# Performance work log

Hardware: AMD Instinct MI355X
Metric: run time of the kernel (lower is better)

The kernel has to match this reference:

```python
import jax, jax.numpy as jnp
import numpy as np
import math

HEAD_DIM = 128
N_HEADS = 32
N_KV_HEADS = 8
HIDDEN = 4096
ROPE_BASE = 10000.0


def _rope_cos_sin(position_ids):
    # inv_freq: [D/2]
    inv_freq = 1.0 / (ROPE_BASE ** (jnp.arange(0, HEAD_DIM, 2, dtype=jnp.float32) / HEAD_DIM))
    freqs = position_ids.astype(jnp.float32)[..., None] * inv_freq  # [B,S,D/2]
    emb = jnp.concatenate([freqs, freqs], axis=-1)  # [B,S,D]
    return jnp.cos(emb), jnp.sin(emb)


def _rotate_half(x):
    x1, x2 = jnp.split(x, 2, axis=-1)
    return jnp.concatenate([-x2, x1], axis=-1)


def setup_inputs() -> dict:
    key = jax.random.key(0)
    ks = jax.random.split(key, 5)
    B, S = 1, 2048
    inp = {
        "hidden_states": jax.random.normal(ks[0], (B, S, HIDDEN), dtype=jnp.float32),
        "position_ids": jnp.arange(B * S, dtype=jnp.int32).reshape(B, S),
        "Wq": jax.random.normal(ks[1], (HIDDEN, N_HEADS * HEAD_DIM), dtype=jnp.float32) * 0.02,
        "Wk": jax.random.normal(ks[2], (HIDDEN, N_KV_HEADS * HEAD_DIM), dtype=jnp.float32) * 0.02,
        "Wv": jax.random.normal(ks[3], (HIDDEN, N_KV_HEADS * HEAD_DIM), dtype=jnp.float32) * 0.02,
        "Wo": jax.random.normal(ks[4], (N_HEADS * HEAD_DIM, HIDDEN), dtype=jnp.float32) * 0.02,
    }
    return inp


def reference(hidden_states, position_ids, Wq, Wk, Wv, Wo):
    B, S, _ = hidden_states.shape
    G = N_HEADS // N_KV_HEADS

    q = (hidden_states @ Wq).reshape(B, S, N_HEADS, HEAD_DIM).transpose(0, 2, 1, 3)      # [B,H,S,D]
    k = (hidden_states @ Wk).reshape(B, S, N_KV_HEADS, HEAD_DIM).transpose(0, 2, 1, 3)   # [B,Hkv,S,D]
    v = (hidden_states @ Wv).reshape(B, S, N_KV_HEADS, HEAD_DIM).transpose(0, 2, 1, 3)

    cos, sin = _rope_cos_sin(position_ids)          # [B,S,D]
    cos = cos[:, None, :, :]                         # [B,1,S,D]
    sin = sin[:, None, :, :]
    q = q * cos + _rotate_half(q) * sin
    k = k * cos + _rotate_half(k) * sin

    # GQA head expansion (repeat_interleave over head dim)
    k = jnp.repeat(k, G, axis=1)                     # [B,H,S,D]
    v = jnp.repeat(v, G, axis=1)

    scale = 1.0 / math.sqrt(HEAD_DIM)
    scores = jnp.einsum("bhqd,bhkd->bhqk", q, k) * scale  # [B,H,S,S]
    causal = jnp.triu(jnp.full((S, S), -jnp.inf, dtype=scores.dtype), k=1)
    scores = scores + causal[None, None]
    probs = jax.nn.softmax(scores.astype(jnp.float32), axis=-1).astype(q.dtype)
    ctx = jnp.einsum("bhqk,bhkd->bhqd", probs, v)    # [B,H,S,D]
    ctx = ctx.transpose(0, 2, 1, 3).reshape(B, S, N_HEADS * HEAD_DIM)
    return ctx @ Wo
```

## Files before the change

### kernel.cpp

```cpp
#include <hip/hip_runtime.h>
#include <hip/hip_bf16.h>
#include <math.h>

#define SEQ 2048
#define NHEADS 32
#define NKVH 8
#define HD 128
#define HIDDEN 4096

typedef unsigned short u16;
typedef unsigned int u32;
typedef __attribute__((ext_vector_type(8))) __bf16 bf16x8;
typedef __attribute__((ext_vector_type(4))) float f32x4;
typedef __attribute__((ext_vector_type(16))) float f32x16;
typedef __attribute__((ext_vector_type(4))) u16 u16x4;
typedef __attribute__((ext_vector_type(4))) u32 u32x4;

__device__ __forceinline__ u16 f2bf(float f) {
  u32 u = __builtin_bit_cast(u32, f);
  u32 r = (u + 0x7fffu + ((u >> 16) & 1u)) >> 16;
  return (u16)r;
}
__device__ __forceinline__ float bf2f(u16 h) {
  return __builtin_bit_cast(float, ((u32)h) << 16);
}
__device__ __forceinline__ void gload_lds16(const void* g, void* l) {
  __builtin_amdgcn_global_load_lds(
      (const __attribute__((address_space(1))) u32*)g,
      (__attribute__((address_space(3))) u32*)l, 16, 0, 0);
}

#define BAR __builtin_amdgcn_s_barrier()
#define PRIO1 __builtin_amdgcn_s_setprio(1)
#define PRIO0 __builtin_amdgcn_s_setprio(0)
#define VMW(n) asm volatile("s_waitcnt vmcnt(" #n ")" ::: "memory")

__global__ void __launch_bounds__(256) prep_all(
    const float* __restrict__ hs, u16* __restrict__ Xb,
    const float* __restrict__ Wq, u16* __restrict__ Wqt,
    const float* __restrict__ Wk, u16* __restrict__ Wkt,
    const float* __restrict__ Wv, u16* __restrict__ Wvt) {
  const int bid = blockIdx.x;
  if (bid < 8192) {
    const int i = (bid * 256 + threadIdx.x) * 4;
    const float4 v = *(const float4*)(hs + i);
    u16x4 o;
    o.x = f2bf(v.x); o.y = f2bf(v.y); o.z = f2bf(v.z); o.w = f2bf(v.w);
    *(u16x4*)(Xb + i) = o;
    return;
  }
  __shared__ float tile[64][65];
  const float* src; u16* dst; int C, lc, tb;
  const int b2 = bid - 8192;
  if (b2 < 4096) { src = Wq; dst = Wqt; C = 4096; lc = 6; tb = b2; }
  else if (b2 < 5120) { src = Wk; dst = Wkt; C = 1024; lc = 4; tb = b2 - 4096; }
  else { src = Wv; dst = Wvt; C = 1024; lc = 4; tb = b2 - 5120; }
  const int r0 = (tb >> lc) * 64, c0 = (tb & ((1 << lc) - 1)) * 64;
  const int tx = threadIdx.x & 63, ty = threadIdx.x >> 6;
#pragma unroll
  for (int j = 0; j < 16; ++j)
    tile[ty + j * 4][tx] = src[(size_t)(r0 + ty + j * 4) * C + c0 + tx];
  __syncthreads();
#pragma unroll
  for (int j = 0; j < 16; ++j)
    dst[(size_t)(c0 + ty + j * 4) * 4096 + r0 + tx] = f2bf(tile[tx][ty + j * 4]);
}

__global__ void __launch_bounds__(256) post_qkv(u16* __restrict__ qb, u16* __restrict__ kb,
                                                const u16* __restrict__ vb, u16* __restrict__ vtb,
                                                const int* __restrict__ pos) {
  const int bid = blockIdx.x;
  if (bid < 20480) {
    u16* x; int lognh; float oscale;
    int idx;
    if (bid < 16384) {
      x = qb; lognh = 5;
      oscale = 0.08838834764831845f * 1.44269504088896340f;
      idx = bid * 256 + threadIdx.x;
    } else {
      x = kb; lognh = 3; oscale = 1.0f;
      idx = (bid - 16384) * 256 + threadIdx.x;
    }
    const int j = idx & 63;
    const int hh = (idx >> 6) & ((1 << lognh) - 1);
    const int s = idx >> (6 + lognh);
    if (s >= SEQ) return;
    const float p = (float)pos[s];
    const float invf = __expf((float)j * -0.14391156831212787f);
    const float ang = p * invf;
    const float c = cosf(ang), sn = sinf(ang);
    u16* bp = x + ((size_t)s << (7 + lognh)) + hh * 128 + j;
    const float x1 = bf2f(bp[0]), x2 = bf2f(bp[64]);
    bp[0] = f2bf((x1 * c - x2 * sn) * oscale);
    bp[64] = f2bf((x2 * c + x1 * sn) * oscale);
    return;
  }
  __shared__ u16 tile[32][34];
  const int b2 = bid - 20480;
  const int c0 = (b2 & 31) * 32, r0 = (b2 >> 5) * 32;
  const int tx = threadIdx.x & 31, ty = threadIdx.x >> 5;
#pragma unroll
  for (int i = 0; i < 4; ++i)
    tile[ty + i * 8][tx] = vb[(size_t)(r0 + ty + i * 8) * 1024 + c0 + tx];
  __syncthreads();
#pragma unroll
  for (int i = 0; i < 4; ++i)
    vtb[(size_t)(c0 + ty + i * 8) * 2048 + r0 + tx] = tile[tx][ty + i * 8];
}

template <int MH, int NH>
__device__ __forceinline__ void mfq32(f32x16 (&acc)[4][2], const bf16x8 (&afr)[2][4],
                                      const bf16x8 (&b)[4]) {
#pragma unroll
  for (int f = 0; f < 2; ++f)
#pragma unroll
    for (int ks = 0; ks < 4; ++ks)
      acc[MH * 2 + f][NH] = __builtin_amdgcn_mfma_f32_32x32x16_bf16(
          afr[f][ks], b[ks], acc[MH * 2 + f][NH], 0, 0, 0);
}

__global__ void __launch_bounds__(512, 2) gemm8p32(
    const u16* __restrict__ A, const u16* __restrict__ B0q, const u16* __restrict__ B1q,
    const u16* __restrict__ B2q, u16* __restrict__ C0, u16* __restrict__ C1,
    u16* __restrict__ C2, const float* __restrict__ Wsrc, u16* __restrict__ Wdst) {
  __shared__ u16 As[2][2][128 * 64];
  __shared__ u16 Bs[2][2][128 * 64];
  const int t = threadIdx.x;
  const int flat = blockIdx.x;
  const int xcd = flat & 7, idx = flat >> 3;

  if (idx >= 24) {
    const int wid = xcd * 8 + (idx - 24);
    float* tf = (float*)&As[0][0][0];
    const int tx = t & 63, ty = t >> 6;
    const int r0 = wid * 64;
    for (int ct = 0; ct < 64; ++ct) {
      const int c0 = ct * 64;
#pragma unroll
      for (int i = 0; i < 8; ++i)
        tf[(ty + i * 8) * 65 + tx] = Wsrc[(size_t)(r0 + ty + i * 8) * 4096 + c0 + tx];
      __syncthreads();
#pragma unroll
      for (int i = 0; i < 8; ++i)
        Wdst[(size_t)(c0 + ty + i * 8) * 4096 + r0 + tx] = f2bf(tf[tx * 65 + ty + i * 8]);
      __syncthreads();
    }
    return;
  }

  const int lane = t & 63, w = t >> 6;
  const int wr = w >> 2, wc = w & 3;
  const int l31 = lane & 31, l5 = lane >> 5;

  int bxt = idx;
  const int byt = xcd;
  const u16* Bp; u16* Cw; int Nn;
  if (bxt < 16) { Bp = B0q; Cw = C0; Nn = 4096; }
  else if (bxt < 20) { bxt -= 16; Bp = B1q; Cw = C1; Nn = 1024; }
  else { bxt -= 20; Bp = B2q; Cw = C2; Nn = 1024; }
  const int row0 = byt * 256, col0 = bxt * 256;

  auto stageA = [&](int buf, int half, int tile) {
#pragma unroll
    for (int g = 0; g < 2; ++g) {
      const int o = (g * 512 + t) * 16;
      const int ridx = o >> 7;
      const int slot = (o >> 4) & 7;
      const int gr = (ridx >> 6) * 128 + half * 64 + (ridx & 63);
      gload_lds16(A + (size_t)(row0 + gr) * 4096 + (tile << 6) + ((slot ^ (ridx & 7)) << 3),
                  (char*)&As[buf][half][0] + o);
    }
  };
  auto stageB = [&](int buf, int half, int tile) {
#pragma unroll
    for (int g = 0; g < 2; ++g) {
      const int o = (g * 512 + t) * 16;
      const int ridx = o >> 7;
      const int slot = (o >> 4) & 7;
      const int gn = (ridx >> 5) * 64 + half * 32 + (ridx & 31);
      gload_lds16(Bp + (size_t)(col0 + gn) * 4096 + (tile << 6) + ((slot ^ (ridx & 7)) << 3),
                  (char*)&Bs[buf][half][0] + o);
    }
  };

  bf16x8 afr[2][4], bf0[4], bf1[4];
  auto loadA32 = [&](int buf, int half) {
#pragma unroll
    for (int f = 0; f < 2; ++f)
#pragma unroll
      for (int ks = 0; ks < 4; ++ks) {
        const int idx2 = wr * 64 + f * 32 + l31;
        const int slot = ks * 2 + l5;
        afr[f][ks] = *(const bf16x8*)((const char*)&As[buf][half][0] + idx2 * 128 +
                                      ((slot ^ (idx2 & 7)) << 4));
      }
  };
  auto loadB32 = [&](int buf, int half, bf16x8 (&dst)[4]) {
#pragma unroll
    for (int ks = 0; ks < 4; ++ks) {
      const int idx2 = wc * 32 + l31;
      const int slot = ks * 2 + l5;
      dst[ks] = *(const bf16x8*)((const char*)&Bs[buf][half][0] + idx2 * 128 +
                                 ((slot ^ (idx2 & 7)) << 4));
    }
  };

  f32x16 acc[4][2];
#pragma unroll
  for (int m_ = 0; m_ < 4; ++m_)
#pragma unroll
    for (int n_ = 0; n_ < 2; ++n_)
#pragma unroll
      for (int e = 0; e < 16; ++e) acc[m_][n_][e] = 0.f;

  const int nit = (4096 >> 6) >> 1;

  stageA(0, 0, 0); stageB(0, 0, 0); stageB(0, 1, 0); stageA(0, 1, 0);
  stageA(1, 0, 1); stageB(1, 0, 1); stageB(1, 1, 1); stageA(1, 1, 1);
  VMW(8);
  BAR;

  for (int i = 0; i < nit; ++i) {
    const int tb = 2 * i;
    const bool g2 = (i + 1 < nit);
    loadA32(0, 0); loadB32(0, 0, bf0);
    BAR; PRIO1; mfq32<0, 0>(acc, afr, bf0); PRIO0; BAR;
    loadB32(0, 1, bf1);
    if (g2) { stageA(0, 0, tb + 2); stageB(0, 0, tb + 2); }
    BAR; PRIO1; mfq32<0, 1>(acc, afr, bf1); PRIO0; BAR;
    loadA32(0, 1);
    if (g2) stageB(0, 1, tb + 2);
    BAR; PRIO1; mfq32<1, 1>(acc, afr, bf1); PRIO0; BAR;
    if (g2) stageA(0, 1, tb + 2);
    BAR; PRIO1; mfq32<1, 0>(acc, afr, bf0); PRIO0;
    if (g2) { VMW(8); } else { VMW(0); }
    BAR;
    loadA32(1, 0); loadB32(1, 0, bf0);
    BAR; PRIO1; mfq32<0, 0>(acc, afr, bf0); PRIO0; BAR;
    loadB32(1, 1, bf1);
    if (g2) { stageA(1, 0, tb + 3); stageB(1, 0, tb + 3); }
    BAR; PRIO1; mfq32<0, 1>(acc, afr, bf1); PRIO0; BAR;
    loadA32(1, 1);
    if (g2) stageB(1, 1, tb + 3);
    BAR; PRIO1; mfq32<1, 1>(acc, afr, bf1); PRIO0; BAR;
    if (g2) stageA(1, 1, tb + 3);
    BAR; PRIO1; mfq32<1, 0>(acc, afr, bf0); PRIO0;
    if (g2) { VMW(8); }
    BAR;
  }

#pragma unroll
  for (int am = 0; am < 4; ++am)
#pragma unroll
    for (int an = 0; an < 2; ++an) {
      const int colb = col0 + wc * 64 + an * 32 + l31;
#pragma unroll
      for (int q = 0; q < 4; ++q) {
        const int rowb = row0 + wr * 128 + am * 32 + q * 8 + l5 * 4;
#pragma unroll
        for (int rr = 0; rr < 4; ++rr)
          Cw[(size_t)(rowb + rr) * Nn + colb] = f2bf(acc[am][an][q * 4 + rr]);
      }
    }
}

template <int MH, int NH>
__device__ __forceinline__ void mfq16(f32x4 (&acc)[4][4], const bf16x8 (&af)[2][2],
                                      const bf16x8 (&b)[2][2]) {
#pragma unroll
  for (int f = 0; f < 2; ++f)
#pragma unroll
    for (int e = 0; e < 2; ++e)
#pragma unroll
      for (int ks = 0; ks < 2; ++ks)
        acc[MH * 2 + f][NH * 2 + e] = __builtin_amdgcn_mfma_f32_16x16x32_bf16(
            af[f][ks], b[e][ks], acc[MH * 2 + f][NH * 2 + e], 0, 0, 0);
}

__global__ void __launch_bounds__(512, 2) gemm8p16(
    const u16* __restrict__ A, const u16* __restrict__ B, float* __restrict__ C) {
  __shared__ u16 As[2][2][64 * 64];
  __shared__ u16 Bs[2][2][128 * 64];
  const int t = threadIdx.x;
  const int lane = t & 63, w = t >> 6;
  const int wr = w >> 2, wc = w & 3;
  const int l15 = lane & 15, l4 = lane >> 4;

  const int flat = blockIdx.x;
  const int xcd = flat & 7, idx = flat >> 3;
  const int bxt = idx & 15, byt = xcd * 2 + (idx >> 4);
  const int row0 = byt * 128, col0 = bxt * 256;

  auto stageA = [&](int buf, int half, int tile) {
    const int o = t * 16;
    const int ridx = o >> 7;
    const int slot = (o >> 4) & 7;
    const int gr = (ridx >> 5) * 64 + half * 32 + (ridx & 31);
    gload_lds16(A + (size_t)(row0 + gr) * 4096 + (tile << 6) + ((slot ^ (ridx & 7)) << 3),
                (char*)&As[buf][half][0] + o);
  };
  auto stageB = [&](int buf, int half, int tile) {
#pragma unroll
    for (int g = 0; g < 2; ++g) {
      const int o = (g * 512 + t) * 16;
      const int ridx = o >> 7;
      const int slot = (o >> 4) & 7;
      const int gn = (ridx >> 5) * 64 + half * 32 + (ridx & 31);
      gload_lds16(B + (size_t)(col0 + gn) * 4096 + (tile << 6) + ((slot ^ (ridx & 7)) << 3),
                  (char*)&Bs[buf][half][0] + o);
    }
  };

  bf16x8 af[2][2], bf0[2][2], bf1[2][2];
  auto loadA = [&](int buf, int half) {
#pragma unroll
    for (int f = 0; f < 2; ++f)
#pragma unroll
      for (int ks = 0; ks < 2; ++ks) {
        const int idx2 = wr * 32 + f * 16 + l15;
        const int slot = ks * 4 + l4;
        af[f][ks] = *(const bf16x8*)((const char*)&As[buf][half][0] + idx2 * 128 +
                                     ((slot ^ (idx2 & 7)) << 4));
      }
  };
  auto loadB = [&](int buf, int half, bf16x8 (&dst)[2][2]) {
#pragma unroll
    for (int e = 0; e < 2; ++e)
#pragma unroll
      for (int ks = 0; ks < 2; ++ks) {
        const int idx2 = wc * 32 + e * 16 + l15;
        const int slot = ks * 4 + l4;
        dst[e][ks] = *(const bf16x8*)((const char*)&Bs[buf][half][0] + idx2 * 128 +
                                      ((slot ^ (idx2 & 7)) << 4));
      }
  };

  f32x4 acc[4][4];
#pragma unroll
  for (int m_ = 0; m_ < 4; ++m_)
#pragma unroll
    for (int n_ = 0; n_ < 4; ++n_) acc[m_][n_] = f32x4{0.f, 0.f, 0.f, 0.f};

  const int nit = (4096 >> 6) >> 1;

  stageA(0, 0, 0); stageB(0, 0, 0); stageB(0, 1, 0); stageA(0, 1, 0);
  stageA(1, 0, 1); stageB(1, 0, 1); stageB(1, 1, 1); stageA(1, 1, 1);
  VMW(6);
  BAR;

  for (int i = 0; i < nit; ++i) {
    const int tb = 2 * i;
    const bool g2 = (i + 1 < nit);
    loadA(0, 0); loadB(0, 0, bf0);
    BAR; PRIO1; mfq16<0, 0>(acc, af, bf0); PRIO0; BAR;
    loadB(0, 1, bf1);
    if (g2) { stageA(0, 0, tb + 2); stageB(0, 0, tb + 2); }
    BAR; PRIO1; mfq16<0, 1>(acc, af, bf1); PRIO0; BAR;
    loadA(0, 1);
    if (g2) stageB(0, 1, tb + 2);
    BAR; PRIO1; mfq16<1, 1>(acc, af, bf1); PRIO0; BAR;
    if (g2) stageA(0, 1, tb + 2);
    BAR; PRIO1; mfq16<1, 0>(acc, af, bf0); PRIO0;
    if (g2) { VMW(6); } else { VMW(0); }
    BAR;
    loadA(1, 0); loadB(1, 0, bf0);
    BAR; PRIO1; mfq16<0, 0>(acc, af, bf0); PRIO0; BAR;
    loadB(1, 1, bf1);
    if (g2) { stageA(1, 0, tb + 3); stageB(1, 0, tb + 3); }
    BAR; PRIO1; mfq16<0, 1>(acc, af, bf1); PRIO0; BAR;
    loadA(1, 1);
    if (g2) stageB(1, 1, tb + 3);
    BAR; PRIO1; mfq16<1, 1>(acc, af, bf1); PRIO0; BAR;
    if (g2) stageA(1, 1, tb + 3);
    BAR; PRIO1; mfq16<1, 0>(acc, af, bf0); PRIO0;
    if (g2) { VMW(6); }
    BAR;
  }

#pragma unroll
  for (int am = 0; am < 4; ++am) {
    const int rowb = row0 + wr * 64 + (am >> 1) * 32 + (am & 1) * 16 + l4 * 4;
#pragma unroll
    for (int an = 0; an < 4; ++an) {
      const int colb = col0 + wc * 64 + (an >> 1) * 32 + (an & 1) * 16 + l15;
#pragma unroll
      for (int r = 0; r < 4; ++r)
        C[(size_t)(rowb + r) * 4096 + colb] = acc[am][an][r];
    }
  }
}

__device__ __forceinline__ void stage_kv512(const u16* __restrict__ k, const u16* __restrict__ vt,
                                            const int kvh, const int kv0, u16* KsB, u16* VsB,
                                            const int t) {
#pragma unroll
  for (int i = 0; i < 2; ++i) {
    const int o = (i * 512 + t) * 16;
    const int row = o >> 8;
    const int slot = (o >> 4) & 15;
    gload_lds16(k + (size_t)(kv0 + row) * (NKVH * HD) + kvh * HD + ((slot ^ (row & 7)) << 3),
                (char*)KsB + o);
  }
#pragma unroll
  for (int i = 0; i < 2; ++i) {
    const int o = (i * 512 + t) * 16;
    const int row = o >> 7;
    const int slot = (o >> 4) & 7;
    gload_lds16(vt + (size_t)(kvh * HD + row) * SEQ + kv0 + ((slot ^ (row & 7)) << 3),
                (char*)VsB + o);
  }
}

__global__ void __launch_bounds__(512) attn_fwd(const u16* __restrict__ q, const u16* __restrict__ k,
                                                const u16* __restrict__ vt, u16* __restrict__ ctx) {
  __shared__ u16 Ks[2][64 * 128];
  __shared__ u16 Vs[2][128 * 64];
  const int t = threadIdx.x, lane = t & 63, w = t >> 6;
  const int bid = blockIdx.x;
  const int xcd = bid & 7, bi = bid >> 3;
  const int h = xcd * 4 + (bi & 3);
  const int qbb = 15 - (bi >> 2);
  const int kvh = xcd;
  const int q0 = qbb * 128;
  const int sq_base = q0 + w * 16;
  const int l15 = lane & 15, l4 = lane >> 4;
  const int sq_abs = sq_base + l15;
  const int bw = sq_base >> 6;

  bf16x8 qf[4];
  {
    const u16* qp = q + (size_t)sq_abs * (NHEADS * HD) + h * HD + l4 * 8;
#pragma unroll
    for (int kb = 0; kb < 4; ++kb) qf[kb] = *(const bf16x8*)(qp + kb * 32);
  }
  f32x4 po[8];
#pragma unroll
  for (int i = 0; i < 8; ++i) po[i] = f32x4{0.f, 0.f, 0.f, 0.f};
  float mrow = -1e30f;
  float lrow = 0.f;

  const int nb = 2 * qbb + 2;
  stage_kv512(k, vt, kvh, 0, Ks[0], Vs[0], t);
  __syncthreads();
  int cur = 0;

  for (int b = 0; b < nb; ++b) {
    if (b + 1 < nb) stage_kv512(k, vt, kvh, (b + 1) * 64, Ks[cur ^ 1], Vs[cur ^ 1], t);

    if (b <= bw) {
      f32x4 st[4];
#pragma unroll
      for (int c = 0; c < 4; ++c) st[c] = f32x4{0.f, 0.f, 0.f, 0.f};
#pragma unroll
      for (int c = 0; c < 4; ++c) {
        const int row = c * 16 + l15;
#pragma unroll
        for (int kb = 0; kb < 4; ++kb) {
          const int slot = kb * 4 + l4;
          bf16x8 bk = *(const bf16x8*)((const char*)Ks[cur] + row * 256 + ((slot ^ (row & 7)) << 4));
          st[c] = __builtin_amdgcn_mfma_f32_16x16x32_bf16(bk, qf[kb], st[c], 0, 0, 0);
        }
      }

      if (b == bw) {
#pragma unroll
        for (int c = 0; c < 4; ++c)
#pragma unroll
          for (int r = 0; r < 4; ++r) {
            const int sk = b * 64 + c * 16 + l4 * 4 + r;
            if (sk > sq_abs) st[c][r] = -1e30f;
          }
      }

      float rmax = -3e38f;
#pragma unroll
      for (int c = 0; c < 4; ++c)
        rmax = fmaxf(rmax, fmaxf(fmaxf(st[c][0], st[c][1]), fmaxf(st[c][2], st[c][3])));
      rmax = fmaxf(rmax, __shfl_xor(rmax, 16, 64));
      rmax = fmaxf(rmax, __shfl_xor(rmax, 32, 64));

      const bool skip = __all(rmax <= mrow + 8.f);
      const float mnew = skip ? mrow : fmaxf(mrow, rmax);

      float rs = 0.f;
#pragma unroll
      for (int c = 0; c < 4; ++c) {
        const float e0 = exp2f(st[c][0] - mnew), e1 = exp2f(st[c][1] - mnew);
        const float e2 = exp2f(st[c][2] - mnew), e3 = exp2f(st[c][3] - mnew);
        st[c][0] = e0; st[c][1] = e1; st[c][2] = e2; st[c][3] = e3;
        rs += (e0 + e1) + (e2 + e3);
      }
      rs += __shfl_xor(rs, 16, 64);
      rs += __shfl_xor(rs, 32, 64);

      if (!skip) {
        const float alpha = exp2f(mrow - mnew);
        mrow = mnew;
        lrow = lrow * alpha + rs;
        float av[4];
#pragma unroll
        for (int r = 0; r < 4; ++r) av[r] = __shfl(alpha, l4 * 4 + r, 16);
#pragma unroll
        for (int db = 0; db < 8; ++db)
#pragma unroll
          for (int r = 0; r < 4; ++r) po[db][r] *= av[r];
      } else {
        lrow += rs;
      }

      u32 pk[4][2];
#pragma unroll
      for (int c = 0; c < 4; ++c) {
        pk[c][0] = (u32)f2bf(st[c][0]) | ((u32)f2bf(st[c][1]) << 16);
        pk[c][1] = (u32)f2bf(st[c][2]) | ((u32)f2bf(st[c][3]) << 16);
      }
      const int src01 = l15 + ((lane & 16) << 1);
      const int src23 = src01 + 16;
      const bool lo = (lane & 32) == 0;
#pragma unroll
      for (int kb2 = 0; kb2 < 2; ++kb2) {
        const int c0 = kb2 * 2, c1 = c0 + 1;
        const u32 a0 = (u32)__shfl((int)pk[c0][0], src01, 64);
        const u32 a1 = (u32)__shfl((int)pk[c0][1], src01, 64);
        const u32 a2 = (u32)__shfl((int)pk[c0][0], src23, 64);
        const u32 a3 = (u32)__shfl((int)pk[c0][1], src23, 64);
        const u32 b0 = (u32)__shfl((int)pk[c1][0], src01, 64);
        const u32 b1 = (u32)__shfl((int)pk[c1][1], src01, 64);
        const u32 b2 = (u32)__shfl((int)pk[c1][0], src23, 64);
        const u32 b3 = (u32)__shfl((int)pk[c1][1], src23, 64);
        u32x4 wq;
        wq.x = lo ? a0 : b0;
        wq.y = lo ? a1 : b1;
        wq.z = lo ? a2 : b2;
        wq.w = lo ? a3 : b3;
        const bf16x8 pa = __builtin_bit_cast(bf16x8, wq);
#pragma unroll
        for (int db = 0; db < 8; ++db) {
          const int vrow = db * 16 + l15;
          const int pslot = kb2 * 4 + l4;
          bf16x8 bv =
              *(const bf16x8*)((const char*)Vs[cur] + vrow * 128 + ((pslot ^ (vrow & 7)) << 4));
          po[db] = __builtin_amdgcn_mfma_f32_16x16x32_bf16(pa, bv, po[db], 0, 0, 0);
        }
      }
    }
    __syncthreads();
    cur ^= 1;
  }

  float rl[4];
#pragma unroll
  for (int r = 0; r < 4; ++r) rl[r] = 1.f / __shfl(lrow, l4 * 4 + r, 16);
#pragma unroll
  for (int db = 0; db < 8; ++db)
#pragma unroll
    for (int r = 0; r < 4; ++r) {
      const int sq = sq_base + l4 * 4 + r;
      const int d = db * 16 + l15;
      ctx[(size_t)sq * (NHEADS * HD) + h * HD + d] = f2bf(po[db][r] * rl[r]);
    }
}

extern "C" void kernel_launch(void* const* d_in, const int* in_sizes, int n_in,
                              void* d_out, int out_size, void* d_ws, size_t ws_size,
                              hipStream_t stream) {
  const float* hs = (const float*)d_in[0];
  const int* pos = (const int*)d_in[1];
  const float* Wq = (const float*)d_in[2];
  const float* Wk = (const float*)d_in[3];
  const float* Wv = (const float*)d_in[4];
  const float* Wo = (const float*)d_in[5];

  u16* ws = (u16*)d_ws;
  u16* Xb = ws;
  u16* Wqt = Xb + (size_t)2048 * 4096;
  u16* Wkt = Wqt + (size_t)4096 * 4096;
  u16* Wvt = Wkt + (size_t)1024 * 4096;
  u16* Wot = Wvt + (size_t)1024 * 4096;
  u16* qb = Wot + (size_t)4096 * 4096;
  u16* kb = qb + (size_t)2048 * 4096;
  u16* vb = kb + (size_t)2048 * 1024;
  u16* vtb = vb + (size_t)2048 * 1024;
  u16* ctx = vtb + (size_t)1024 * 2048;
  const size_t need = ((size_t)(ctx - ws) + (size_t)2048 * 4096) * 2;
  if (ws_size < need) return;

  prep_all<<<14336, 256, 0, stream>>>(hs, Xb, Wq, Wqt, Wk, Wkt, Wv, Wvt);

  gemm8p32<<<256, 512, 0, stream>>>(Xb, Wqt, Wkt, Wvt, qb, kb, vb, Wo, Wot);

  post_qkv<<<22528, 256, 0, stream>>>(qb, kb, vb, vtb, pos);

  attn_fwd<<<512, 512, 0, stream>>>(qb, kb, vtb, ctx);

  gemm8p16<<<256, 512, 0, stream>>>(ctx, Wot, (float*)d_out);
}
```

Measured before the change: 338.4 us.

## Replace both GEMM kernels with a unified 128x128-tile double-buffered kernel

Both the QKV projection GEMM (previously 256x256 tiles with 32x32 MFMA) and the output projection GEMM (128x256 tiles) are replaced by one templated kernel. It uses 128x128 tiles, 16x16x32 MFMA, a simple two-buffer K-loop and a launch bound of 4 blocks per CU. Smaller tiles give more blocks (768 and 512) for better CU fill and occupancy. The cost is lower arithmetic intensity per block, more global and LDS traffic, and a simpler schedule that loses the fine-grained interleaving of loads and MFMAs. The Wo transpose blocks are now launched after the GEMM blocks.

Measured after the change: 365.1 us. 1.08x slower.

```diff
diff --git a/kernel.cpp b/kernel.cpp
--- a/kernel.cpp
+++ b/kernel.cpp
@@ -12,7 +12,6 @@
 typedef unsigned int u32;
 typedef __attribute__((ext_vector_type(8))) __bf16 bf16x8;
 typedef __attribute__((ext_vector_type(4))) float f32x4;
-typedef __attribute__((ext_vector_type(16))) float f32x16;
 typedef __attribute__((ext_vector_type(4))) u16 u16x4;
 typedef __attribute__((ext_vector_type(4))) u32 u32x4;
 
@@ -34,6 +33,7 @@
 #define PRIO1 __builtin_amdgcn_s_setprio(1)
 #define PRIO0 __builtin_amdgcn_s_setprio(0)
 #define VMW(n) asm volatile("s_waitcnt vmcnt(" #n ")" ::: "memory")
+#define LGKM0 asm volatile("s_waitcnt lgkmcnt(0)" ::: "memory")
 
 __global__ void __launch_bounds__(256) prep_all(
     const float* __restrict__ hs, u16* __restrict__ Xb,
@@ -108,30 +108,21 @@
     vtb[(size_t)(c0 + ty + i * 8) * 2048 + r0 + tx] = tile[tx][ty + i * 8];
 }
 
-template <int MH, int NH>
-__device__ __forceinline__ void mfq32(f32x16 (&acc)[4][2], const bf16x8 (&afr)[2][4],
-                                      const bf16x8 (&b)[4]) {
-#pragma unroll
-  for (int f = 0; f < 2; ++f)
-#pragma unroll
-    for (int ks = 0; ks < 4; ++ks)
-      acc[MH * 2 + f][NH] = __builtin_amdgcn_mfma_f32_32x32x16_bf16(
-          afr[f][ks], b[ks], acc[MH * 2 + f][NH], 0, 0, 0);
-}
-
-__global__ void __launch_bounds__(512, 2) gemm8p32(
+template <int WRITE_F32>
+__global__ void __launch_bounds__(512, 4) gemm2p(
     const u16* __restrict__ A, const u16* __restrict__ B0q, const u16* __restrict__ B1q,
-    const u16* __restrict__ B2q, u16* __restrict__ C0, u16* __restrict__ C1,
-    u16* __restrict__ C2, const float* __restrict__ Wsrc, u16* __restrict__ Wdst) {
-  __shared__ u16 As[2][2][128 * 64];
-  __shared__ u16 Bs[2][2][128 * 64];
+    const u16* __restrict__ B2q, void* __restrict__ C0, void* __restrict__ C1,
+    void* __restrict__ C2, const int K, const int n0t, const int n1t,
+    const int N0, const int N1, const int N2, const int ncol,
+    const float* __restrict__ Wsrc, u16* __restrict__ Wdst, const int ngemm) {
+  __shared__ u16 As[2][128 * 64];
+  __shared__ u16 Bs[2][128 * 64];
   const int t = threadIdx.x;
-  const int flat = blockIdx.x;
-  const int xcd = flat & 7, idx = flat >> 3;
-
-  if (idx >= 24) {
-    const int wid = xcd * 8 + (idx - 24);
-    float* tf = (float*)&As[0][0][0];
+  const int bid = blockIdx.x;
+
+  if (bid >= ngemm) {
+    const int wid = bid - ngemm;
+    float* tf = (float*)&As[0][0];
     const int tx = t & 63, ty = t >> 6;
     const int r0 = wid * 64;
     for (int ct = 0; ct < 64; ++ct) {
@@ -150,242 +141,110 @@
 
   const int lane = t & 63, w = t >> 6;
   const int wr = w >> 2, wc = w & 3;
-  const int l31 = lane & 31, l5 = lane >> 5;
-
-  int bxt = idx;
-  const int byt = xcd;
-  const u16* Bp; u16* Cw; int Nn;
-  if (bxt < 16) { Bp = B0q; Cw = C0; Nn = 4096; }
-  else if (bxt < 20) { bxt -= 16; Bp = B1q; Cw = C1; Nn = 1024; }
-  else { bxt -= 20; Bp = B2q; Cw = C2; Nn = 1024; }
-  const int row0 = byt * 256, col0 = bxt * 256;
-
-  auto stageA = [&](int buf, int half, int tile) {
+  const int l15 = lane & 15, l4 = lane >> 4;
+
+  const int xcd = bid & 7, ii = bid >> 3;
+  int bxt = ii % ncol;
+  const int byt = xcd * 2 + ii / ncol;
+  const u16* Bp; char* Cw; int Nn;
+  if (bxt < n0t) { Bp = B0q; Cw = (char*)C0; Nn = N0; }
+  else if (bxt < n0t + n1t) { bxt -= n0t; Bp = B1q; Cw = (char*)C1; Nn = N1; }
+  else { bxt -= n0t + n1t; Bp = B2q; Cw = (char*)C2; Nn = N2; }
+  const int row0 = byt * 128, col0 = bxt * 128;
+
+  auto stageAB = [&](int buf, int tile) {
 #pragma unroll
     for (int g = 0; g < 2; ++g) {
       const int o = (g * 512 + t) * 16;
       const int ridx = o >> 7;
       const int slot = (o >> 4) & 7;
-      const int gr = (ridx >> 6) * 128 + half * 64 + (ridx & 63);
-      gload_lds16(A + (size_t)(row0 + gr) * 4096 + (tile << 6) + ((slot ^ (ridx & 7)) << 3),
-                  (char*)&As[buf][half][0] + o);
-    }
-  };
-  auto stageB = [&](int buf, int half, int tile) {
+      gload_lds16(A + (size_t)(row0 + ridx) * K + (tile << 6) + ((slot ^ (ridx & 7)) << 3),
+                  (char*)&As[buf][0] + o);
+    }
 #pragma unroll
     for (int g = 0; g < 2; ++g) {
       const int o = (g * 512 + t) * 16;
       const int ridx = o >> 7;
       const int slot = (o >> 4) & 7;
-      const int gn = (ridx >> 5) * 64 + half * 32 + (ridx & 31);
-      gload_lds16(Bp + (size_t)(col0 + gn) * 4096 + (tile << 6) + ((slot ^ (ridx & 7)) << 3),
-                  (char*)&Bs[buf][half][0] + o);
+      gload_lds16(Bp + (size_t)(col0 + ridx) * K + (tile << 6) + ((slot ^ (ridx & 7)) << 3),
+                  (char*)&Bs[buf][0] + o);
     }
   };
 
-  bf16x8 afr[2][4], bf0[4], bf1[4];
-  auto loadA32 = [&](int buf, int half) {
-#pragma unroll
-    for (int f = 0; f < 2; ++f)
-#pragma unroll
-      for (int ks = 0; ks < 4; ++ks) {
-        const int idx2 = wr * 64 + f * 32 + l31;
-        const int slot = ks * 2 + l5;
-        afr[f][ks] = *(const bf16x8*)((const char*)&As[buf][half][0] + idx2 * 128 +
-                                      ((slot ^ (idx2 & 7)) << 4));
+  bf16x8 af[4][2], bf[2][2];
+  auto loadA = [&](int buf) {
+#pragma unroll
+    for (int f = 0; f < 4; ++f)
+#pragma unroll
+      for (int ks = 0; ks < 2; ++ks) {
+        const int idx2 = wr * 64 + f * 16 + l15;
+        const int slot = ks * 4 + l4;
+        af[f][ks] = *(const bf16x8*)((const char*)&As[buf][0] + idx2 * 128 +
+                                     ((slot ^ (idx2 & 7)) << 4));
       }
   };
-  auto loadB32 = [&](int buf, int half, bf16x8 (&dst)[4]) {
-#pragma unroll
-    for (int ks = 0; ks < 4; ++ks) {
-      const int idx2 = wc * 32 + l31;
-      const int slot = ks * 2 + l5;
-      dst[ks] = *(const bf16x8*)((const char*)&Bs[buf][half][0] + idx2 * 128 +
-                                 ((slot ^ (idx2 & 7)) << 4));
-    }
-  };
-
-  f32x16 acc[4][2];
-#pragma unroll
-  for (int m_ = 0; m_ < 4; ++m_)
-#pragma unroll
-    for (int n_ = 0; n_ < 2; ++n_)
-#pragma unroll
-      for (int e = 0; e < 16; ++e) acc[m_][n_][e] = 0.f;
-
-  const int nit = (4096 >> 6) >> 1;
-
-  stageA(0, 0, 0); stageB(0, 0, 0); stageB(0, 1, 0); stageA(0, 1, 0);
-  stageA(1, 0, 1); stageB(1, 0, 1); stageB(1, 1, 1); stageA(1, 1, 1);
-  VMW(8);
-  BAR;
-
-  for (int i = 0; i < nit; ++i) {
-    const int tb = 2 * i;
-    const bool g2 = (i + 1 < nit);
-    loadA32(0, 0); loadB32(0, 0, bf0);
-    BAR; PRIO1; mfq32<0, 0>(acc, afr, bf0); PRIO0; BAR;
-    loadB32(0, 1, bf1);
-    if (g2) { stageA(0, 0, tb + 2); stageB(0, 0, tb + 2); }
-    BAR; PRIO1; mfq32<0, 1>(acc, afr, bf1); PRIO0; BAR;
-    loadA32(0, 1);
-    if (g2) stageB(0, 1, tb + 2);
-    BAR; PRIO1; mfq32<1, 1>(acc, afr, bf1); PRIO0; BAR;
-    if (g2) stageA(0, 1, tb + 2);
-    BAR; PRIO1; mfq32<1, 0>(acc, afr, bf0); PRIO0;
-    if (g2) { VMW(8); } else { VMW(0); }
-    BAR;
-    loadA32(1, 0); loadB32(1, 0, bf0);
-    BAR; PRIO1; mfq32<0, 0>(acc, afr, bf0); PRIO0; BAR;
-    loadB32(1, 1, bf1);
-    if (g2) { stageA(1, 0, tb + 3); stageB(1, 0, tb + 3); }
-    BAR; PRIO1; mfq32<0, 1>(acc, afr, bf1); PRIO0; BAR;
-    loadA32(1, 1);
-    if (g2) stageB(1, 1, tb + 3);
-    BAR; PRIO1; mfq32<1, 1>(acc, afr, bf1); PRIO0; BAR;
-    if (g2) stageA(1, 1, tb + 3);
-    BAR; PRIO1; mfq32<1, 0>(acc, afr, bf0); PRIO0;
-    if (g2) { VMW(8); }
-    BAR;
-  }
-
-#pragma unroll
-  for (int am = 0; am < 4; ++am)
-#pragma unroll
-    for (int an = 0; an < 2; ++an) {
-      const int colb = col0 + wc * 64 + an * 32 + l31;
-#pragma unroll
-      for (int q = 0; q < 4; ++q) {
-        const int rowb = row0 + wr * 128 + am * 32 + q * 8 + l5 * 4;
-#pragma unroll
-        for (int rr = 0; rr < 4; ++rr)
-          Cw[(size_t)(rowb + rr) * Nn + colb] = f2bf(acc[am][an][q * 4 + rr]);
-      }
-    }
-}
-
-template <int MH, int NH>
-__device__ __forceinline__ void mfq16(f32x4 (&acc)[4][4], const bf16x8 (&af)[2][2],
-                                      const bf16x8 (&b)[2][2]) {
-#pragma unroll
-  for (int f = 0; f < 2; ++f)
-#pragma unroll
-    for (int e = 0; e < 2; ++e)
-#pragma unroll
-      for (int ks = 0; ks < 2; ++ks)
-        acc[MH * 2 + f][NH * 2 + e] = __builtin_amdgcn_mfma_f32_16x16x32_bf16(
-            af[f][ks], b[e][ks], acc[MH * 2 + f][NH * 2 + e], 0, 0, 0);
-}
-
-__global__ void __launch_bounds__(512, 2) gemm8p16(
-    const u16* __restrict__ A, const u16* __restrict__ B, float* __restrict__ C) {
-  __shared__ u16 As[2][2][64 * 64];
-  __shared__ u16 Bs[2][2][128 * 64];
-  const int t = threadIdx.x;
-  const int lane = t & 63, w = t >> 6;
-  const int wr = w >> 2, wc = w & 3;
-  const int l15 = lane & 15, l4 = lane >> 4;
-
-  const int flat = blockIdx.x;
-  const int xcd = flat & 7, idx = flat >> 3;
-  const int bxt = idx & 15, byt = xcd * 2 + (idx >> 4);
-  const int row0 = byt * 128, col0 = bxt * 256;
-
-  auto stageA = [&](int buf, int half, int tile) {
-    const int o = t * 16;
-    const int ridx = o >> 7;
-    const int slot = (o >> 4) & 7;
-    const int gr = (ridx >> 5) * 64 + half * 32 + (ridx & 31);
-    gload_lds16(A + (size_t)(row0 + gr) * 4096 + (tile << 6) + ((slot ^ (ridx & 7)) << 3),
-                (char*)&As[buf][half][0] + o);
-  };
-  auto stageB = [&](int buf, int half, int tile) {
-#pragma unroll
-    for (int g = 0; g < 2; ++g) {
-      const int o = (g * 512 + t) * 16;
-      const int ridx = o >> 7;
-      const int slot = (o >> 4) & 7;
-      const int gn = (ridx >> 5) * 64 + half * 32 + (ridx & 31);
-      gload_lds16(B + (size_t)(col0 + gn) * 4096 + (tile << 6) + ((slot ^ (ridx & 7)) << 3),
-                  (char*)&Bs[buf][half][0] + o);
-    }
-  };
-
-  bf16x8 af[2][2], bf0[2][2], bf1[2][2];
-  auto loadA = [&](int buf, int half) {
-#pragma unroll
-    for (int f = 0; f < 2; ++f)
-#pragma unroll
-      for (int ks = 0; ks < 2; ++ks) {
-        const int idx2 = wr * 32 + f * 16 + l15;
-        const int slot = ks * 4 + l4;
-        af[f][ks] = *(const bf16x8*)((const char*)&As[buf][half][0] + idx2 * 128 +
-                                     ((slot ^ (idx2 & 7)) << 4));
-      }
-  };
-  auto loadB = [&](int buf, int half, bf16x8 (&dst)[2][2]) {
+  auto loadB = [&](int buf) {
 #pragma unroll
     for (int e = 0; e < 2; ++e)
 #pragma unroll
       for (int ks = 0; ks < 2; ++ks) {
         const int idx2 = wc * 32 + e * 16 + l15;
         const int slot = ks * 4 + l4;
-        dst[e][ks] = *(const bf16x8*)((const char*)&Bs[buf][half][0] + idx2 * 128 +
-                                      ((slot ^ (idx2 & 7)) << 4));
+        bf[e][ks] = *(const bf16x8*)((const char*)&Bs[buf][0] + idx2 * 128 +
+                                     ((slot ^ (idx2 & 7)) << 4));
       }
   };
 
-  f32x4 acc[4][4];
-#pragma unroll
-  for (int m_ = 0; m_ < 4; ++m_)
-#pragma unroll
-    for (int n_ = 0; n_ < 4; ++n_) acc[m_][n_] = f32x4{0.f, 0.f, 0.f, 0.f};
-
-  const int nit = (4096 >> 6) >> 1;
-
-  stageA(0, 0, 0); stageB(0, 0, 0); stageB(0, 1, 0); stageA(0, 1, 0);
-  stageA(1, 0, 1); stageB(1, 0, 1); stageB(1, 1, 1); stageA(1, 1, 1);
-  VMW(6);
+  f32x4 acc[4][2];
+#pragma unroll
+  for (int f = 0; f < 4; ++f)
+#pragma unroll
+    for (int e = 0; e < 2; ++e) acc[f][e] = f32x4{0.f, 0.f, 0.f, 0.f};
+
+  const int nkt = K >> 6;
+
+  stageAB(0, 0);
+  stageAB(1, 1);
+  VMW(4);
   BAR;
 
-  for (int i = 0; i < nit; ++i) {
-    const int tb = 2 * i;
-    const bool g2 = (i + 1 < nit);
-    loadA(0, 0); loadB(0, 0, bf0);
-    BAR; PRIO1; mfq16<0, 0>(acc, af, bf0); PRIO0; BAR;
-    loadB(0, 1, bf1);
-    if (g2) { stageA(0, 0, tb + 2); stageB(0, 0, tb + 2); }
-    BAR; PRIO1; mfq16<0, 1>(acc, af, bf1); PRIO0; BAR;
-    loadA(0, 1);
-    if (g2) stageB(0, 1, tb + 2);
-    BAR; PRIO1; mfq16<1, 1>(acc, af, bf1); PRIO0; BAR;
-    if (g2) stageA(0, 1, tb + 2);
-    BAR; PRIO1; mfq16<1, 0>(acc, af, bf0); PRIO0;
-    if (g2) { VMW(6); } else { VMW(0); }
+  for (int kt = 0; kt < nkt; ++kt) {
+    const int buf = kt & 1;
+    loadA(buf); loadB(buf);
+    LGKM0;
     BAR;
-    loadA(1, 0); loadB(1, 0, bf0);
-    BAR; PRIO1; mfq16<0, 0>(acc, af, bf0); PRIO0; BAR;
-    loadB(1, 1, bf1);
-    if (g2) { stageA(1, 0, tb + 3); stageB(1, 0, tb + 3); }
-    BAR; PRIO1; mfq16<0, 1>(acc, af, bf1); PRIO0; BAR;
-    loadA(1, 1);
-    if (g2) stageB(1, 1, tb + 3);
-    BAR; PRIO1; mfq16<1, 1>(acc, af, bf1); PRIO0; BAR;
-    if (g2) stageA(1, 1, tb + 3);
-    BAR; PRIO1; mfq16<1, 0>(acc, af, bf0); PRIO0;
-    if (g2) { VMW(6); }
+    if (kt + 2 < nkt) stageAB(buf, kt + 2);
+    PRIO1;
+#pragma unroll
+    for (int f = 0; f < 4; ++f)
+#pragma unroll
+      for (int e = 0; e < 2; ++e)
+#pragma unroll
+        for (int ks = 0; ks < 2; ++ks)
+          acc[f][e] = __builtin_amdgcn_mfma_f32_16x16x32_bf16(af[f][ks], bf[e][ks], acc[f][e],
+                                                              0, 0, 0);
+    PRIO0;
+    if (kt + 2 < nkt) { VMW(4); } else { VMW(0); }
     BAR;
   }
 
 #pragma unroll
-  for (int am = 0; am < 4; ++am) {
-    const int rowb = row0 + wr * 64 + (am >> 1) * 32 + (am & 1) * 16 + l4 * 4;
-#pragma unroll
-    for (int an = 0; an < 4; ++an) {
-      const int colb = col0 + wc * 64 + (an >> 1) * 32 + (an & 1) * 16 + l15;
-#pragma unroll
-      for (int r = 0; r < 4; ++r)
-        C[(size_t)(rowb + r) * 4096 + colb] = acc[am][an][r];
+  for (int f = 0; f < 4; ++f) {
+    const int rowb = row0 + wr * 64 + f * 16 + l4 * 4;
+#pragma unroll
+    for (int e = 0; e < 2; ++e) {
+      const int colb = col0 + wc * 32 + e * 16 + l15;
+      if (WRITE_F32) {
+        float* C = (float*)Cw;
+#pragma unroll
+        for (int r = 0; r < 4; ++r)
+          C[(size_t)(rowb + r) * Nn + colb] = acc[f][e][r];
+      } else {
+        u16* C = (u16*)Cw;
+#pragma unroll
+        for (int r = 0; r < 4; ++r)
+          C[(size_t)(rowb + r) * Nn + colb] = f2bf(acc[f][e][r]);
+      }
     }
   }
 }
@@ -587,11 +446,13 @@
 
   prep_all<<<14336, 256, 0, stream>>>(hs, Xb, Wq, Wqt, Wk, Wkt, Wv, Wvt);
 
-  gemm8p32<<<256, 512, 0, stream>>>(Xb, Wqt, Wkt, Wvt, qb, kb, vb, Wo, Wot);
+  gemm2p<0><<<832, 512, 0, stream>>>(Xb, Wqt, Wkt, Wvt, qb, kb, vb,
+                                     4096, 32, 8, 4096, 1024, 1024, 48, Wo, Wot, 768);
 
   post_qkv<<<22528, 256, 0, stream>>>(qb, kb, vb, vtb, pos);
 
   attn_fwd<<<512, 512, 0, stream>>>(qb, kb, vtb, ctx);
 
-  gemm8p16<<<256, 512, 0, stream>>>(ctx, Wot, (float*)d_out);
-}
+  gemm2p<1><<<512, 512, 0, stream>>>(ctx, Wot, Wot, Wot, d_out, d_out, d_out,
+                                     4096, 32, 0, 4096, 4096, 4096, 32, nullptr, nullptr, 512);
+}
```

## Fuse QKV into one GEMM with 256x192 tiles and move Wo transpose into attention

Applied to the files above, without the earlier changes.

Replaces the QKV GEMM, which used three separate outputs, 256x256 tiles and 32x32 MFMA, with a single GEMM writing a packed [S,6144] QKV buffer. It uses 256x192 tiles, 16x16x32 MFMA and a new single-tile-per-step pipeline. This relies on Wqt, Wkt and Wv being laid out contiguously. The Wo transpose/convert blocks move from the GEMM launch into extra blocks of the attention kernel, so they can overlap with attention work instead of occupying GEMM slots. The post-processing and attention kernels are updated for the packed layout.

Measured after the change: 330.0 us. -2.5%, faster.

```diff
diff --git a/kernel.cpp b/kernel.cpp
--- a/kernel.cpp
+++ b/kernel.cpp
@@ -7,12 +7,12 @@
 #define NKVH 8
 #define HD 128
 #define HIDDEN 4096
+#define NQKV 6144
 
 typedef unsigned short u16;
 typedef unsigned int u32;
 typedef __attribute__((ext_vector_type(8))) __bf16 bf16x8;
 typedef __attribute__((ext_vector_type(4))) float f32x4;
-typedef __attribute__((ext_vector_type(16))) float f32x16;
 typedef __attribute__((ext_vector_type(4))) u16 u16x4;
 typedef __attribute__((ext_vector_type(4))) u32 u32x4;
 
@@ -66,30 +66,31 @@
     dst[(size_t)(c0 + ty + j * 4) * 4096 + r0 + tx] = f2bf(tile[tx][ty + j * 4]);
 }
 
-__global__ void __launch_bounds__(256) post_qkv(u16* __restrict__ qb, u16* __restrict__ kb,
-                                                const u16* __restrict__ vb, u16* __restrict__ vtb,
+__global__ void __launch_bounds__(256) post_qkv(u16* __restrict__ qkv, u16* __restrict__ vtb,
                                                 const int* __restrict__ pos) {
   const int bid = blockIdx.x;
   if (bid < 20480) {
-    u16* x; int lognh; float oscale;
-    int idx;
+    int idx, hoff, sshift;
+    float oscale;
     if (bid < 16384) {
-      x = qb; lognh = 5;
+      idx = bid * 256 + threadIdx.x;
+      hoff = ((idx >> 6) & 31) * 128;
+      sshift = 11;
       oscale = 0.08838834764831845f * 1.44269504088896340f;
-      idx = bid * 256 + threadIdx.x;
     } else {
-      x = kb; lognh = 3; oscale = 1.0f;
       idx = (bid - 16384) * 256 + threadIdx.x;
+      hoff = 4096 + ((idx >> 6) & 7) * 128;
+      sshift = 9;
+      oscale = 1.0f;
     }
     const int j = idx & 63;
-    const int hh = (idx >> 6) & ((1 << lognh) - 1);
-    const int s = idx >> (6 + lognh);
+    const int s = idx >> sshift;
     if (s >= SEQ) return;
     const float p = (float)pos[s];
     const float invf = __expf((float)j * -0.14391156831212787f);
     const float ang = p * invf;
     const float c = cosf(ang), sn = sinf(ang);
-    u16* bp = x + ((size_t)s << (7 + lognh)) + hh * 128 + j;
+    u16* bp = qkv + (size_t)s * NQKV + hoff + j;
     const float x1 = bf2f(bp[0]), x2 = bf2f(bp[64]);
     bp[0] = f2bf((x1 * c - x2 * sn) * oscale);
     bp[64] = f2bf((x2 * c + x1 * sn) * oscale);
@@ -101,166 +102,135 @@
   const int tx = threadIdx.x & 31, ty = threadIdx.x >> 5;
 #pragma unroll
   for (int i = 0; i < 4; ++i)
-    tile[ty + i * 8][tx] = vb[(size_t)(r0 + ty + i * 8) * 1024 + c0 + tx];
+    tile[ty + i * 8][tx] = qkv[(size_t)(r0 + ty + i * 8) * NQKV + 5120 + c0 + tx];
   __syncthreads();
 #pragma unroll
   for (int i = 0; i < 4; ++i)
     vtb[(size_t)(c0 + ty + i * 8) * 2048 + r0 + tx] = tile[tx][ty + i * 8];
 }
 
-template <int MH, int NH>
-__device__ __forceinline__ void mfq32(f32x16 (&acc)[4][2], const bf16x8 (&afr)[2][4],
-                                      const bf16x8 (&b)[4]) {
-#pragma unroll
-  for (int f = 0; f < 2; ++f)
-#pragma unroll
-    for (int ks = 0; ks < 4; ++ks)
-      acc[MH * 2 + f][NH] = __builtin_amdgcn_mfma_f32_32x32x16_bf16(
-          afr[f][ks], b[ks], acc[MH * 2 + f][NH], 0, 0, 0);
-}
-
-__global__ void __launch_bounds__(512, 2) gemm8p32(
-    const u16* __restrict__ A, const u16* __restrict__ B0q, const u16* __restrict__ B1q,
-    const u16* __restrict__ B2q, u16* __restrict__ C0, u16* __restrict__ C1,
-    u16* __restrict__ C2, const float* __restrict__ Wsrc, u16* __restrict__ Wdst) {
-  __shared__ u16 As[2][2][128 * 64];
-  __shared__ u16 Bs[2][2][128 * 64];
+__global__ void __launch_bounds__(512) gemm_qkv(
+    const u16* __restrict__ A, const u16* __restrict__ B, u16* __restrict__ C) {
+  __shared__ u16 As[2][256 * 64];
+  __shared__ u16 Bs[2][192 * 64];
   const int t = threadIdx.x;
-  const int flat = blockIdx.x;
-  const int xcd = flat & 7, idx = flat >> 3;
-
-  if (idx >= 24) {
-    const int wid = xcd * 8 + (idx - 24);
-    float* tf = (float*)&As[0][0][0];
-    const int tx = t & 63, ty = t >> 6;
-    const int r0 = wid * 64;
-    for (int ct = 0; ct < 64; ++ct) {
-      const int c0 = ct * 64;
-#pragma unroll
-      for (int i = 0; i < 8; ++i)
-        tf[(ty + i * 8) * 65 + tx] = Wsrc[(size_t)(r0 + ty + i * 8) * 4096 + c0 + tx];
-      __syncthreads();
-#pragma unroll
-      for (int i = 0; i < 8; ++i)
-        Wdst[(size_t)(c0 + ty + i * 8) * 4096 + r0 + tx] = f2bf(tf[tx * 65 + ty + i * 8]);
-      __syncthreads();
-    }
-    return;
-  }
-
   const int lane = t & 63, w = t >> 6;
   const int wr = w >> 2, wc = w & 3;
-  const int l31 = lane & 31, l5 = lane >> 5;
-
-  int bxt = idx;
-  const int byt = xcd;
-  const u16* Bp; u16* Cw; int Nn;
-  if (bxt < 16) { Bp = B0q; Cw = C0; Nn = 4096; }
-  else if (bxt < 20) { bxt -= 16; Bp = B1q; Cw = C1; Nn = 1024; }
-  else { bxt -= 20; Bp = B2q; Cw = C2; Nn = 1024; }
-  const int row0 = byt * 256, col0 = bxt * 256;
-
-  auto stageA = [&](int buf, int half, int tile) {
-#pragma unroll
-    for (int g = 0; g < 2; ++g) {
+  const int l15 = lane & 15, l4 = lane >> 4;
+
+  const int bid = blockIdx.x;
+  const int xcd = bid & 7, ii = bid >> 3;
+  const int byt = xcd, bxt = ii;
+  const int row0 = byt * 256, col0 = bxt * 192;
+
+  auto stageA_part = [&](int buf, int tile, int gfirst) {
+#pragma unroll
+    for (int gg = 0; gg < 2; ++gg) {
+      const int g = gfirst + gg * 2;
       const int o = (g * 512 + t) * 16;
       const int ridx = o >> 7;
       const int slot = (o >> 4) & 7;
-      const int gr = (ridx >> 6) * 128 + half * 64 + (ridx & 63);
-      gload_lds16(A + (size_t)(row0 + gr) * 4096 + (tile << 6) + ((slot ^ (ridx & 7)) << 3),
-                  (char*)&As[buf][half][0] + o);
-    }
-  };
-  auto stageB = [&](int buf, int half, int tile) {
-#pragma unroll
-    for (int g = 0; g < 2; ++g) {
+      gload_lds16(A + (size_t)(row0 + ridx) * 4096 + (tile << 6) + ((slot ^ (ridx & 7)) << 3),
+                  (char*)&As[buf][0] + o);
+    }
+  };
+  auto stageB = [&](int buf, int tile) {
+#pragma unroll
+    for (int g = 0; g < 3; ++g) {
       const int o = (g * 512 + t) * 16;
       const int ridx = o >> 7;
       const int slot = (o >> 4) & 7;
-      const int gn = (ridx >> 5) * 64 + half * 32 + (ridx & 31);
-      gload_lds16(Bp + (size_t)(col0 + gn) * 4096 + (tile << 6) + ((slot ^ (ridx & 7)) << 3),
-                  (char*)&Bs[buf][half][0] + o);
-    }
-  };
-
-  bf16x8 afr[2][4], bf0[4], bf1[4];
-  auto loadA32 = [&](int buf, int half) {
-#pragma unroll
-    for (int f = 0; f < 2; ++f)
-#pragma unroll
-      for (int ks = 0; ks < 4; ++ks) {
-        const int idx2 = wr * 64 + f * 32 + l31;
-        const int slot = ks * 2 + l5;
-        afr[f][ks] = *(const bf16x8*)((const char*)&As[buf][half][0] + idx2 * 128 +
+      gload_lds16(B + (size_t)(col0 + ridx) * 4096 + (tile << 6) + ((slot ^ (ridx & 7)) << 3),
+                  (char*)&Bs[buf][0] + o);
+    }
+  };
+
+  bf16x8 af[4][2], bfr[3][2];
+  auto loadA = [&](int buf, int mh) {
+#pragma unroll
+    for (int f = 0; f < 4; ++f)
+#pragma unroll
+      for (int ks = 0; ks < 2; ++ks) {
+        const int idx2 = wr * 128 + mh * 64 + f * 16 + l15;
+        const int slot = ks * 4 + l4;
+        af[f][ks] = *(const bf16x8*)((const char*)&As[buf][0] + idx2 * 128 +
+                                     ((slot ^ (idx2 & 7)) << 4));
+      }
+  };
+  auto loadB = [&](int buf) {
+#pragma unroll
+    for (int e = 0; e < 3; ++e)
+#pragma unroll
+      for (int ks = 0; ks < 2; ++ks) {
+        const int idx2 = wc * 48 + e * 16 + l15;
+        const int slot = ks * 4 + l4;
+        bfr[e][ks] = *(const bf16x8*)((const char*)&Bs[buf][0] + idx2 * 128 +
                                       ((slot ^ (idx2 & 7)) << 4));
       }
   };
-  auto loadB32 = [&](int buf, int half, bf16x8 (&dst)[4]) {
-#pragma unroll
-    for (int ks = 0; ks < 4; ++ks) {
-      const int idx2 = wc * 32 + l31;
-      const int slot = ks * 2 + l5;
-      dst[ks] = *(const bf16x8*)((const char*)&Bs[buf][half][0] + idx2 * 128 +
-                                 ((slot ^ (idx2 & 7)) << 4));
-    }
-  };
-
-  f32x16 acc[4][2];
-#pragma unroll
-  for (int m_ = 0; m_ < 4; ++m_)
-#pragma unroll
-    for (int n_ = 0; n_ < 2; ++n_)
-#pragma unroll
-      for (int e = 0; e < 16; ++e) acc[m_][n_][e] = 0.f;
-
-  const int nit = (4096 >> 6) >> 1;
-
-  stageA(0, 0, 0); stageB(0, 0, 0); stageB(0, 1, 0); stageA(0, 1, 0);
-  stageA(1, 0, 1); stageB(1, 0, 1); stageB(1, 1, 1); stageA(1, 1, 1);
-  VMW(8);
+
+  f32x4 acc0[4][3], acc1[4][3];
+#pragma unroll
+  for (int f = 0; f < 4; ++f)
+#pragma unroll
+    for (int e = 0; e < 3; ++e) {
+      acc0[f][e] = f32x4{0.f, 0.f, 0.f, 0.f};
+      acc1[f][e] = f32x4{0.f, 0.f, 0.f, 0.f};
+    }
+
+  const int nkt = 4096 >> 6;
+
+  stageA_part(0, 0, 0); stageA_part(0, 0, 1); stageB(0, 0);
+  stageA_part(1, 1, 0); stageA_part(1, 1, 1); stageB(1, 1);
+  VMW(7);
   BAR;
 
-  for (int i = 0; i < nit; ++i) {
-    const int tb = 2 * i;
-    const bool g2 = (i + 1 < nit);
-    loadA32(0, 0); loadB32(0, 0, bf0);
-    BAR; PRIO1; mfq32<0, 0>(acc, afr, bf0); PRIO0; BAR;
-    loadB32(0, 1, bf1);
-    if (g2) { stageA(0, 0, tb + 2); stageB(0, 0, tb + 2); }
-    BAR; PRIO1; mfq32<0, 1>(acc, afr, bf1); PRIO0; BAR;
-    loadA32(0, 1);
-    if (g2) stageB(0, 1, tb + 2);
-    BAR; PRIO1; mfq32<1, 1>(acc, afr, bf1); PRIO0; BAR;
-    if (g2) stageA(0, 1, tb + 2);
-    BAR; PRIO1; mfq32<1, 0>(acc, afr, bf0); PRIO0;
-    if (g2) { VMW(8); } else { VMW(0); }
+  for (int kt = 0; kt < nkt; ++kt) {
+    const int buf = kt & 1;
+    loadA(buf, 0); loadB(buf);
+    if (kt >= 1 && kt + 1 < nkt) { stageA_part(buf ^ 1, kt + 1, 1); stageB(buf ^ 1, kt + 1); }
     BAR;
-    loadA32(1, 0); loadB32(1, 0, bf0);
-    BAR; PRIO1; mfq32<0, 0>(acc, afr, bf0); PRIO0; BAR;
-    loadB32(1, 1, bf1);
-    if (g2) { stageA(1, 0, tb + 3); stageB(1, 0, tb + 3); }
-    BAR; PRIO1; mfq32<0, 1>(acc, afr, bf1); PRIO0; BAR;
-    loadA32(1, 1);
-    if (g2) stageB(1, 1, tb + 3);
-    BAR; PRIO1; mfq32<1, 1>(acc, afr, bf1); PRIO0; BAR;
-    if (g2) stageA(1, 1, tb + 3);
-    BAR; PRIO1; mfq32<1, 0>(acc, afr, bf0); PRIO0;
-    if (g2) { VMW(8); }
+    PRIO1;
+#pragma unroll
+    for (int f = 0; f < 4; ++f)
+#pragma unroll
+      for (int e = 0; e < 3; ++e)
+#pragma unroll
+        for (int ks = 0; ks < 2; ++ks)
+          acc0[f][e] = __builtin_amdgcn_mfma_f32_16x16x32_bf16(af[f][ks], bfr[e][ks], acc0[f][e],
+                                                               0, 0, 0);
+    PRIO0;
     BAR;
-  }
-
-#pragma unroll
-  for (int am = 0; am < 4; ++am)
-#pragma unroll
-    for (int an = 0; an < 2; ++an) {
-      const int colb = col0 + wc * 64 + an * 32 + l31;
-#pragma unroll
-      for (int q = 0; q < 4; ++q) {
-        const int rowb = row0 + wr * 128 + am * 32 + q * 8 + l5 * 4;
-#pragma unroll
-        for (int rr = 0; rr < 4; ++rr)
-          Cw[(size_t)(rowb + rr) * Nn + colb] = f2bf(acc[am][an][q * 4 + rr]);
-      }
+    loadA(buf, 1);
+    if (kt + 2 < nkt) stageA_part(buf, kt + 2, 0);
+    BAR;
+    PRIO1;
+#pragma unroll
+    for (int f = 0; f < 4; ++f)
+#pragma unroll
+      for (int e = 0; e < 3; ++e)
+#pragma unroll
+        for (int ks = 0; ks < 2; ++ks)
+          acc1[f][e] = __builtin_amdgcn_mfma_f32_16x16x32_bf16(af[f][ks], bfr[e][ks], acc1[f][e],
+                                                               0, 0, 0);
+    PRIO0;
+    if (kt + 2 < nkt) { VMW(2); } else { VMW(0); }
+    BAR;
+  }
+
+#pragma unroll
+  for (int f = 0; f < 4; ++f)
+#pragma unroll
+    for (int e = 0; e < 3; ++e) {
+      const int colb = col0 + wc * 48 + e * 16 + l15;
+      const int r0a = row0 + wr * 128 + f * 16 + l4 * 4;
+#pragma unroll
+      for (int r = 0; r < 4; ++r)
+        C[(size_t)(r0a + r) * NQKV + colb] = f2bf(acc0[f][e][r]);
+      const int r0b = r0a + 64;
+#pragma unroll
+      for (int r = 0; r < 4; ++r)
+        C[(size_t)(r0b + r) * NQKV + colb] = f2bf(acc1[f][e][r]);
     }
 }
 
@@ -390,7 +360,7 @@
   }
 }
 
-__device__ __forceinline__ void stage_kv512(const u16* __restrict__ k, const u16* __restrict__ vt,
+__device__ __forceinline__ void stage_kv512(const u16* __restrict__ qkv, const u16* __restrict__ vt,
                                             const int kvh, const int kv0, u16* KsB, u16* VsB,
                                             const int t) {
 #pragma unroll
@@ -398,7 +368,7 @@
     const int o = (i * 512 + t) * 16;
     const int row = o >> 8;
     const int slot = (o >> 4) & 15;
-    gload_lds16(k + (size_t)(kv0 + row) * (NKVH * HD) + kvh * HD + ((slot ^ (row & 7)) << 3),
+    gload_lds16(qkv + (size_t)(kv0 + row) * NQKV + 4096 + kvh * HD + ((slot ^ (row & 7)) << 3),
                 (char*)KsB + o);
   }
 #pragma unroll
@@ -411,12 +381,34 @@
   }
 }
 
-__global__ void __launch_bounds__(512) attn_fwd(const u16* __restrict__ q, const u16* __restrict__ k,
-                                                const u16* __restrict__ vt, u16* __restrict__ ctx) {
+__global__ void __launch_bounds__(512) attn_fwd(const u16* __restrict__ qkv,
+                                                const u16* __restrict__ vt, u16* __restrict__ ctx,
+                                                const float* __restrict__ Wsrc,
+                                                u16* __restrict__ Wdst) {
   __shared__ u16 Ks[2][64 * 128];
   __shared__ u16 Vs[2][128 * 64];
   const int t = threadIdx.x, lane = t & 63, w = t >> 6;
   const int bid = blockIdx.x;
+
+  if (bid >= 512) {
+    const int wid = bid - 512;
+    float* tf = (float*)&Ks[0][0];
+    const int tx = t & 63, ty = t >> 6;
+    const int r0 = wid * 64;
+    for (int ct = 0; ct < 64; ++ct) {
+      const int c0 = ct * 64;
+#pragma unroll
+      for (int i = 0; i < 8; ++i)
+        tf[(ty + i * 8) * 65 + tx] = Wsrc[(size_t)(r0 + ty + i * 8) * 4096 + c0 + tx];
+      __syncthreads();
+#pragma unroll
+      for (int i = 0; i < 8; ++i)
+        Wdst[(size_t)(c0 + ty + i * 8) * 4096 + r0 + tx] = f2bf(tf[tx * 65 + ty + i * 8]);
+      __syncthreads();
+    }
+    return;
+  }
+
   const int xcd = bid & 7, bi = bid >> 3;
   const int h = xcd * 4 + (bi & 3);
   const int qbb = 15 - (bi >> 2);
@@ -429,7 +421,7 @@
 
   bf16x8 qf[4];
   {
-    const u16* qp = q + (size_t)sq_abs * (NHEADS * HD) + h * HD + l4 * 8;
+    const u16* qp = qkv + (size_t)sq_abs * NQKV + h * HD + l4 * 8;
 #pragma unroll
     for (int kb = 0; kb < 4; ++kb) qf[kb] = *(const bf16x8*)(qp + kb * 32);
   }
@@ -440,12 +432,12 @@
   float lrow = 0.f;
 
   const int nb = 2 * qbb + 2;
-  stage_kv512(k, vt, kvh, 0, Ks[0], Vs[0], t);
+  stage_kv512(qkv, vt, kvh, 0, Ks[0], Vs[0], t);
   __syncthreads();
   int cur = 0;
 
   for (int b = 0; b < nb; ++b) {
-    if (b + 1 < nb) stage_kv512(k, vt, kvh, (b + 1) * 64, Ks[cur ^ 1], Vs[cur ^ 1], t);
+    if (b + 1 < nb) stage_kv512(qkv, vt, kvh, (b + 1) * 64, Ks[cur ^ 1], Vs[cur ^ 1], t);
 
     if (b <= bw) {
       f32x4 st[4];
@@ -577,21 +569,19 @@
   u16* Wkt = Wqt + (size_t)4096 * 4096;
   u16* Wvt = Wkt + (size_t)1024 * 4096;
   u16* Wot = Wvt + (size_t)1024 * 4096;
-  u16* qb = Wot + (size_t)4096 * 4096;
-  u16* kb = qb + (size_t)2048 * 4096;
-  u16* vb = kb + (size_t)2048 * 1024;
-  u16* vtb = vb + (size_t)2048 * 1024;
+  u16* qkvb = Wot + (size_t)4096 * 4096;
+  u16* vtb = qkvb + (size_t)2048 * 6144;
   u16* ctx = vtb + (size_t)1024 * 2048;
   const size_t need = ((size_t)(ctx - ws) + (size_t)2048 * 4096) * 2;
   if (ws_size < need) return;
 
   prep_all<<<14336, 256, 0, stream>>>(hs, Xb, Wq, Wqt, Wk, Wkt, Wv, Wvt);
 
-  gemm8p32<<<256, 512, 0, stream>>>(Xb, Wqt, Wkt, Wvt, qb, kb, vb, Wo, Wot);
-
-  post_qkv<<<22528, 256, 0, stream>>>(qb, kb, vb, vtb, pos);
-
-  attn_fwd<<<512, 512, 0, stream>>>(qb, kb, vtb, ctx);
+  gemm_qkv<<<256, 512, 0, stream>>>(Xb, Wqt, qkvb);
+
+  post_qkv<<<22528, 256, 0, stream>>>(qkvb, vtb, pos);
+
+  attn_fwd<<<576, 512, 0, stream>>>(qkvb, vtb, ctx, Wo, Wot);
 
   gemm8p16<<<256, 512, 0, stream>>>(ctx, Wot, (float*)d_out);
 }
```
